# Optimization experiments

Hardware: AMD Instinct MI355X
Metric: run time of the kernel (lower is better)

## Reference

```python
import jax, jax.numpy as jnp
import numpy as np

N = 4096      # number of nodes
C = 8         # channels (w1..w8 in source)
IN_DIM = 256  # input feature dim
D = 64        # per-channel dim (c_dim)
OUT = 128     # out_dim
ITERS = 4     # routing iterations
BETA = 1.0    # temperature
DENSITY = 0.01


def _l2norm(x):
    # tf.nn.l2_normalize along last axis with eps=1e-12
    return x * jax.lax.rsqrt(jnp.maximum(jnp.sum(x * x, axis=-1, keepdims=True), 1e-12))


def setup_inputs() -> dict:
    key = jax.random.key(0)
    k0, k1, k2, k3, k4, k5 = jax.random.split(key, 6)
    features = jax.random.normal(k0, (N, IN_DIM), dtype=jnp.float32)
    # sparse-ish 0/1 adjacency stored densely (as in the original model)
    adj = (jax.random.uniform(k1, (N, N)) < DENSITY).astype(jnp.float32)
    W = jax.random.normal(k2, (C, IN_DIM, D), dtype=jnp.float32)    # w1..w8 stacked
    b = jax.random.normal(k3, (C, 1, D), dtype=jnp.float32)         # b1..b8 stacked
    W_o = jax.random.normal(k4, (C * D, OUT), dtype=jnp.float32)
    bias = jax.random.normal(k5, (1, OUT), dtype=jnp.float32)
    return {"features": features, "adj": adj, "W": W, "b": b, "W_o": W_o, "bias": bias}


def reference(features, adj, W, b, W_o, bias):
    mask = adj > 0  # [N, N]
    # per-channel projection + l2 normalize: z[c] = l2norm(features @ w[c] + b[c])
    z = _l2norm(jnp.einsum('ni,cid->cnd', features, W) + b)  # [C, N, D]
    for _ in range(ITERS):
        # dense per-channel attention (XX^T), masked by adjacency
        A = jnp.einsum('cnd,cmd->cnm', z, z)                 # [C, N, N]
        A = jnp.where(mask[None], A, 0.0) / BETA
        # softmax across channels at each (i, j), then re-mask
        A = jax.nn.softmax(A, axis=0)
        A = jnp.where(mask[None], A, 0.0)
        # aggregate + residual + l2 normalize
        z = _l2norm(z + jnp.einsum('cnm,cmd->cnd', A, z))
    # concat channels along feature axis: [N, C*D]
    h = jnp.transpose(z, (1, 0, 2)).reshape(N, C * D)
    # (dropout skipped: stochastic op, identity in the deterministic reference)
    return h @ W_o + bias
```

## Files before the change

### kernel.cpp

```cpp
#include <hip/hip_runtime.h>
#include <hip/hip_bf16.h>

#define N_NODES 4096
#define C_CH    8
#define IN_DIM  256
#define D_DIM   64
#define CD      512
#define OUT_DIM 128
#define ITERS   4
#define STRIDE  128

typedef __hip_bfloat16 bf16;
typedef short short8 __attribute__((ext_vector_type(8)));
typedef float floatx4 __attribute__((ext_vector_type(4)));

__device__ __forceinline__ float bf2f(bf16 x) { return __bfloat162float(x); }

__device__ __forceinline__ unsigned f2b_rne(float x) {
    unsigned u = __float_as_uint(x);
    return (u + 0x7FFFu + ((u >> 16) & 1u)) >> 16;
}
__device__ __forceinline__ unsigned pack2bf(float a, float b) {
    return f2b_rne(a) | (f2b_rne(b) << 16);
}
__device__ __forceinline__ void unpack2(unsigned v, float& a, float& b) {
    a = __uint_as_float(v << 16);
    b = __uint_as_float(v & 0xFFFF0000u);
}
__device__ __forceinline__ short8 as_s8(uint4 u) {
    union { uint4 a; short8 b; } x; x.a = u; return x.b;
}

template<int CTRL>
__device__ __forceinline__ float dpp_add(float x) {
    int yi = __builtin_amdgcn_update_dpp(0, __float_as_int(x), CTRL, 0xF, 0xF, true);
    return x + __int_as_float(yi);
}

__device__ __forceinline__ bool wave_detect(const unsigned* __restrict__ feat_u) {
    int lane = threadIdx.x & 63;
    unsigned u = feat_u[lane];
    int e = (u >> 7) & 0xFF;
    int vote = (e >= 0x68 && e <= 0x86) ? 1 : 0;
    #pragma unroll
    for (int off = 32; off; off >>= 1) vote += __shfl_xor(vote, off);
    return vote >= 32;
}

__global__ __launch_bounds__(256) void stage_a(
        const void* __restrict__ feat, const void* __restrict__ W,
        const void* __restrict__ Wo,
        unsigned short* __restrict__ Wt, unsigned short* __restrict__ Wo_t) {
    bool isbf = wave_detect((const unsigned*)feat);
    int bx = blockIdx.x, t = threadIdx.x;
    if (bx < 8) {
        __shared__ __align__(16) unsigned short lt[IN_DIM * D_DIM];
        int c = bx;
        if (isbf) {
            const uint4* p = (const uint4*)((const unsigned short*)W + (size_t)c * IN_DIM * D_DIM);
            #pragma unroll
            for (int i = 0; i < 8; i++) {
                int idx = t + i * 256;
                *(uint4*)&lt[idx * 8] = p[idx];
            }
        } else {
            const float4* p = (const float4*)((const float*)W + (size_t)c * IN_DIM * D_DIM);
            #pragma unroll
            for (int i = 0; i < 16; i++) {
                int idx = t + i * 256;
                float4 f = p[idx];
                uint2 v = make_uint2(pack2bf(f.x, f.y), pack2bf(f.z, f.w));
                *(uint2*)&lt[idx * 4] = v;
            }
        }
        __syncthreads();
        uint4* wt4 = (uint4*)Wt;
        #pragma unroll
        for (int i = 0; i < 8; i++) {
            int j = t + i * 256;
            int d = j >> 5, seg = j & 31;
            int k0 = seg * 8;
            unsigned short v[8];
            #pragma unroll
            for (int k = 0; k < 8; k++) v[k] = lt[(k0 + k) * D_DIM + d];
            uint4 o;
            o.x = v[0] | ((unsigned)v[1] << 16);
            o.y = v[2] | ((unsigned)v[3] << 16);
            o.z = v[4] | ((unsigned)v[5] << 16);
            o.w = v[6] | ((unsigned)v[7] << 16);
            wt4[(c * 64 + d) * 32 + seg] = o;
        }
    } else {
        int base = (bx - 8) * 1024 + t * 4;
        #pragma unroll
        for (int q = 0; q < 4; q++) {
            int idx = base + q;
            int k = idx >> 7, n = idx & 127;
            unsigned short v;
            if (isbf) v = ((const unsigned short*)Wo)[idx];
            else      v = (unsigned short)f2b_rne(((const float*)Wo)[idx]);
            Wo_t[n * CD + k] = v;
        }
    }
}

__global__ __launch_bounds__(256) void stage_b(
        const void* __restrict__ feat, const void* __restrict__ adj,
        const void* __restrict__ b, const unsigned short* __restrict__ Wt,
        unsigned* __restrict__ zbf, int* __restrict__ deg,
        int* __restrict__ col_buf) {
    bool isbf = wave_detect((const unsigned*)feat);
    int bx = blockIdx.x, t = threadIdx.x;
    int w = t >> 6, lane = t & 63;
    __shared__ __align__(16) unsigned short zt[16 * CD];

    if (bx < 256) {
        int r0 = bx * 16;
        int n0 = w * 128;
        int m = lane & 15, quad = lane >> 4;
        int row = r0 + m;
        floatx4 acc[8];
        #pragma unroll
        for (int j = 0; j < 8; j++) acc[j] = (floatx4){0.f, 0.f, 0.f, 0.f};
        const uint4* wt4 = (const uint4*)Wt;

        if (isbf) {
            const uint4* a4 = (const uint4*)feat + (size_t)row * 32 + quad;
            #pragma unroll
            for (int k0 = 0; k0 < 8; k0++) {
                short8 a = as_s8(a4[k0 * 4]);
                #pragma unroll
                for (int j = 0; j < 8; j++) {
                    int col = n0 + j * 16 + m;
                    short8 bb = as_s8(wt4[col * 32 + k0 * 4 + quad]);
                    acc[j] = __builtin_amdgcn_mfma_f32_16x16x32_bf16(a, bb, acc[j], 0, 0, 0);
                }
            }
        } else {
            const float4* a4 = (const float4*)feat + (size_t)row * 64 + quad * 2;
            #pragma unroll
            for (int k0 = 0; k0 < 8; k0++) {
                float4 f0 = a4[k0 * 8], f1 = a4[k0 * 8 + 1];
                uint4 au;
                au.x = pack2bf(f0.x, f0.y); au.y = pack2bf(f0.z, f0.w);
                au.z = pack2bf(f1.x, f1.y); au.w = pack2bf(f1.z, f1.w);
                short8 a = as_s8(au);
                #pragma unroll
                for (int j = 0; j < 8; j++) {
                    int col = n0 + j * 16 + m;
                    short8 bb = as_s8(wt4[col * 32 + k0 * 4 + quad]);
                    acc[j] = __builtin_amdgcn_mfma_f32_16x16x32_bf16(a, bb, acc[j], 0, 0, 0);
                }
            }
        }

        float pre[8][4];
        #pragma unroll
        for (int j = 0; j < 8; j++) {
            int col = n0 + j * 16 + m;
            float bb = isbf ? bf2f(((const bf16*)b)[col]) : ((const float*)b)[col];
            #pragma unroll
            for (int r = 0; r < 4; r++) pre[j][r] = acc[j][r] + bb;
        }
        #pragma unroll
        for (int ch = 0; ch < 2; ch++) {
            float ss[4];
            #pragma unroll
            for (int r = 0; r < 4; r++) {
                float s = 0.f;
                #pragma unroll
                for (int jj = 0; jj < 4; jj++) {
                    float v = pre[ch * 4 + jj][r];
                    s = fmaf(v, v, s);
                }
                ss[r] = s;
            }
            #pragma unroll
            for (int off = 1; off < 16; off <<= 1) {
                #pragma unroll
                for (int r = 0; r < 4; r++) ss[r] += __shfl_xor(ss[r], off);
            }
            #pragma unroll
            for (int r = 0; r < 4; r++) {
                float sc = __builtin_amdgcn_rsqf(fmaxf(ss[r], 1e-12f));
                int lrow = quad * 4 + r;
                #pragma unroll
                for (int jj = 0; jj < 4; jj++) {
                    int j = ch * 4 + jj;
                    int col = n0 + j * 16 + m;
                    zt[lrow * CD + col] = (unsigned short)f2b_rne(pre[j][r] * sc);
                }
            }
        }
        __syncthreads();
        const uint4* zt4 = (const uint4*)zt;
        uint4* z4 = (uint4*)zbf;
        #pragma unroll
        for (int i = 0; i < 4; i++) {
            int j = t + i * 256;
            int lrow = j >> 6, seg = j & 63;
            z4[(size_t)(r0 + lrow) * 64 + seg] = zt4[j];
        }
    } else {
        int i = (bx - 256) * 4 + w;
        int base_out = i * STRIDE;
        int running = 0;
        int nch = isbf ? 8 : 16;
        for (int ch = 0; ch < nch; ch++) {
            unsigned bits = 0;
            int j0, nelem;
            if (isbf) {
                const uint4* p = (const uint4*)((const unsigned short*)adj + (size_t)i * N_NODES);
                uint4 u = p[ch * 64 + lane];
                j0 = (ch * 64 + lane) * 8; nelem = 8;
                unsigned short h[8] = {
                    (unsigned short)(u.x & 0xFFFF), (unsigned short)(u.x >> 16),
                    (unsigned short)(u.y & 0xFFFF), (unsigned short)(u.y >> 16),
                    (unsigned short)(u.z & 0xFFFF), (unsigned short)(u.z >> 16),
                    (unsigned short)(u.w & 0xFFFF), (unsigned short)(u.w >> 16)};
                #pragma unroll
                for (int k = 0; k < 8; k++)
                    if ((h[k] & 0x8000) == 0 && h[k] != 0) bits |= (1u << k);
            } else {
                const float4* p = (const float4*)((const float*)adj + (size_t)i * N_NODES);
                float4 f = p[ch * 64 + lane];
                j0 = (ch * 64 + lane) * 4; nelem = 4;
                if (f.x > 0.f) bits |= 1u;
                if (f.y > 0.f) bits |= 2u;
                if (f.z > 0.f) bits |= 4u;
                if (f.w > 0.f) bits |= 8u;
            }
            int cnt = __popc(bits);
            int sc = cnt;
            #pragma unroll
            for (int off = 1; off < 64; off <<= 1) {
                int v = __shfl_up(sc, off);
                if (lane >= off) sc += v;
            }
            int tot = __shfl(sc, 63);
            int pos = base_out + running + (sc - cnt);
            for (int k = 0; k < nelem; k++) {
                if ((bits >> k) & 1u) {
                    if (pos < base_out + STRIDE) col_buf[pos] = j0 + k;
                    pos++;
                }
            }
            running += tot;
        }
        if (lane == 0) deg[i] = (running < STRIDE) ? running : STRIDE;
    }
}

__device__ __forceinline__ void edge_step(const float zi[8], float acc[8], uint4 u) {
    float vj[8];
    unpack2(u.x, vj[0], vj[1]);
    unpack2(u.y, vj[2], vj[3]);
    unpack2(u.z, vj[4], vj[5]);
    unpack2(u.w, vj[6], vj[7]);
    float p = 0.f;
    #pragma unroll
    for (int k = 0; k < 8; k++) p = fmaf(zi[k], vj[k], p);
    p = dpp_add<0xB1>(p);
    p = dpp_add<0x4E>(p);
    p = dpp_add<0x141>(p);
    float ex = __expf(p);
    float s = dpp_add<0x128>(ex);
    s += __shfl_xor(s, 16);
    s += __shfl_xor(s, 32);
    float wgt = ex * __builtin_amdgcn_rcpf(s);
    #pragma unroll
    for (int k = 0; k < 8; k++) acc[k] = fmaf(wgt, vj[k], acc[k]);
}

__global__ __launch_bounds__(256) void route_kernel(
        const unsigned* __restrict__ zbf_in, unsigned* __restrict__ zbf_out,
        const int* __restrict__ deg, const int* __restrict__ col_buf) {
    int t = threadIdx.x;
    int w = t >> 6, lane = t & 63;
    int i = blockIdx.x;
    int g = lane >> 3, s = lane & 7;
    __shared__ int   s_cols[STRIDE];
    __shared__ float s_acc[3][CD];
    if (t < STRIDE) s_cols[t] = col_buf[i * STRIDE + t];
    __syncthreads();

    int frag = g * 32 + s * 4;
    uint4 uown = *(const uint4*)(zbf_in + (size_t)i * 256 + frag);
    float zi[8], acc[8];
    unpack2(uown.x, zi[0], zi[1]); unpack2(uown.y, zi[2], zi[3]);
    unpack2(uown.z, zi[4], zi[5]); unpack2(uown.w, zi[6], zi[7]);
    #pragma unroll
    for (int k = 0; k < 8; k++) acc[k] = (w == 0) ? zi[k] : 0.f;

    int dg = deg[i];
    int e   = (dg * w) >> 2;
    int end = (dg * (w + 1)) >> 2;
    for (; e + 3 < end; e += 4) {
        int j0 = s_cols[e]     & (N_NODES - 1);
        int j1 = s_cols[e + 1] & (N_NODES - 1);
        int j2 = s_cols[e + 2] & (N_NODES - 1);
        int j3 = s_cols[e + 3] & (N_NODES - 1);
        uint4 u0 = *(const uint4*)(zbf_in + (size_t)j0 * 256 + frag);
        uint4 u1 = *(const uint4*)(zbf_in + (size_t)j1 * 256 + frag);
        uint4 u2 = *(const uint4*)(zbf_in + (size_t)j2 * 256 + frag);
        uint4 u3 = *(const uint4*)(zbf_in + (size_t)j3 * 256 + frag);
        edge_step(zi, acc, u0);
        edge_step(zi, acc, u1);
        edge_step(zi, acc, u2);
        edge_step(zi, acc, u3);
    }
    for (; e < end; e++) {
        int j0 = s_cols[e] & (N_NODES - 1);
        uint4 u0 = *(const uint4*)(zbf_in + (size_t)j0 * 256 + frag);
        edge_step(zi, acc, u0);
    }

    int flat = g * D_DIM + s * 8;
    if (w) {
        *(float4*)&s_acc[w - 1][flat]     = make_float4(acc[0], acc[1], acc[2], acc[3]);
        *(float4*)&s_acc[w - 1][flat + 4] = make_float4(acc[4], acc[5], acc[6], acc[7]);
    }
    __syncthreads();
    if (w == 0) {
        #pragma unroll
        for (int q = 0; q < 3; q++) {
            float4 p0 = *(const float4*)&s_acc[q][flat];
            float4 p1 = *(const float4*)&s_acc[q][flat + 4];
            acc[0] += p0.x; acc[1] += p0.y; acc[2] += p0.z; acc[3] += p0.w;
            acc[4] += p1.x; acc[5] += p1.y; acc[6] += p1.z; acc[7] += p1.w;
        }
        float ss = 0.f;
        #pragma unroll
        for (int k = 0; k < 8; k++) ss = fmaf(acc[k], acc[k], ss);
        ss = dpp_add<0xB1>(ss);
        ss = dpp_add<0x4E>(ss);
        ss = dpp_add<0x141>(ss);
        float sc = __builtin_amdgcn_rsqf(fmaxf(ss, 1e-12f));
        float o[8];
        #pragma unroll
        for (int k = 0; k < 8; k++) o[k] = acc[k] * sc;
        uint4 ob;
        ob.x = pack2bf(o[0], o[1]); ob.y = pack2bf(o[2], o[3]);
        ob.z = pack2bf(o[4], o[5]); ob.w = pack2bf(o[6], o[7]);
        *(uint4*)(zbf_out + (size_t)i * 256 + frag) = ob;
    }
}

__global__ __launch_bounds__(256) void out_gemm_mfma(
        const unsigned* __restrict__ zbf, const unsigned* __restrict__ wot_u,
        const void* __restrict__ bias, void* __restrict__ out,
        const void* __restrict__ feat) {
    bool isbf = wave_detect((const unsigned*)feat);
    int w = threadIdx.x >> 6, lane = threadIdx.x & 63;
    int r0 = blockIdx.x * 32 + (w & 1) * 16;
    int n0 = (w >> 1) * 64;
    int m = lane & 15, quad = lane >> 4;

    floatx4 acc0 = {0.f, 0.f, 0.f, 0.f}, acc1 = acc0, acc2 = acc0, acc3 = acc0;
    const unsigned* ap  = zbf   + (size_t)(r0 + m) * 256 + quad * 4;
    const unsigned* bp0 = wot_u + (size_t)(n0 + m) * 256 + quad * 4;
    const unsigned* bp1 = bp0 + 16 * 256;
    const unsigned* bp2 = bp0 + 32 * 256;
    const unsigned* bp3 = bp0 + 48 * 256;

    #pragma unroll
    for (int k0 = 0; k0 < 256; k0 += 16) {
        short8 a  = as_s8(*(const uint4*)(ap  + k0));
        short8 b0 = as_s8(*(const uint4*)(bp0 + k0));
        short8 b1 = as_s8(*(const uint4*)(bp1 + k0));
        short8 b2 = as_s8(*(const uint4*)(bp2 + k0));
        short8 b3 = as_s8(*(const uint4*)(bp3 + k0));
        acc0 = __builtin_amdgcn_mfma_f32_16x16x32_bf16(a, b0, acc0, 0, 0, 0);
        acc1 = __builtin_amdgcn_mfma_f32_16x16x32_bf16(a, b1, acc1, 0, 0, 0);
        acc2 = __builtin_amdgcn_mfma_f32_16x16x32_bf16(a, b2, acc2, 0, 0, 0);
        acc3 = __builtin_amdgcn_mfma_f32_16x16x32_bf16(a, b3, acc3, 0, 0, 0);
    }

    float accs[4][4] = {
        {acc0[0], acc0[1], acc0[2], acc0[3]},
        {acc1[0], acc1[1], acc1[2], acc1[3]},
        {acc2[0], acc2[1], acc2[2], acc2[3]},
        {acc3[0], acc3[1], acc3[2], acc3[3]}};
    #pragma unroll
    for (int c = 0; c < 4; c++) {
        int col = n0 + c * 16 + m;
        float bb = isbf ? bf2f(((const bf16*)bias)[col]) : ((const float*)bias)[col];
        #pragma unroll
        for (int r = 0; r < 4; r++) {
            int row = r0 + quad * 4 + r;
            float v = accs[c][r] + bb;
            size_t oi = (size_t)row * OUT_DIM + col;
            if (isbf) ((bf16*)out)[oi] = __float2bfloat16(v);
            else      ((float*)out)[oi] = v;
        }
    }
}

extern "C" void kernel_launch(void* const* d_in, const int* in_sizes, int n_in,
                              void* d_out, int out_size, void* d_ws, size_t ws_size,
                              hipStream_t stream) {
    const void* feat = d_in[0];
    const void* adj  = d_in[1];
    const void* W    = d_in[2];
    const void* b    = d_in[3];
    const void* Wo   = d_in[4];
    const void* bias = d_in[5];

    char* ws = (char*)d_ws;
    unsigned*       zbf_a   = (unsigned*)ws;
    unsigned*       zbf_b   = (unsigned*)(ws + (4u << 20));
    unsigned short* Wt      = (unsigned short*)(ws + (8u << 20));
    unsigned short* Wo_t    = (unsigned short*)(ws + (8u << 20) + (256u << 10));
    int*            deg     = (int*)(ws + (8u << 20) + (512u << 10));
    int*            col_buf = (int*)(ws + (9u << 20));

    stage_a<<<72, 256, 0, stream>>>(feat, W, Wo, Wt, Wo_t);
    stage_b<<<1280, 256, 0, stream>>>(feat, adj, b, Wt, zbf_a, deg, col_buf);

    unsigned* bin = zbf_a;
    unsigned* bot = zbf_b;
    for (int it = 0; it < ITERS; it++) {
        route_kernel<<<N_NODES, 256, 0, stream>>>(bin, bot, deg, col_buf);
        unsigned* tb = bin; bin = bot; bot = tb;
    }
    out_gemm_mfma<<<N_NODES / 32, 256, 0, stream>>>(zbf_a, (const unsigned*)Wo_t,
                                                    bias, d_out, feat);
}
```

Before: 206.1 us.

## Fuse routing iterations into one cooperative kernel with one node per wave

Replaces the four per-iteration route launches with a single cooperative kernel that keeps each node's vector in registers and uses grid-wide syncs between iterations, falling back to per-iteration launches when cooperative launch is not possible. Each wave now handles a whole node instead of four waves splitting one node's edges, which removes the shared-memory partial-sum reduction and the block barrier. It also switches exp to exp2 with a prescaled query and masks column indices once when they are loaded. The trade-offs are grid-sync cost and the occupancy limit (1024 blocks must be co-resident), plus load imbalance from per-node degree now falling on a single wave.

```diff
diff --git a/kernel.cpp b/kernel.cpp
--- a/kernel.cpp
+++ b/kernel.cpp
@@ -1,5 +1,8 @@
 #include <hip/hip_runtime.h>
 #include <hip/hip_bf16.h>
+#include <hip/hip_cooperative_groups.h>
+
+namespace cg = cooperative_groups;
 
 #define N_NODES 4096
 #define C_CH    8
@@ -251,7 +254,7 @@
     }
 }
 
-__device__ __forceinline__ void edge_step(const float zi[8], float acc[8], uint4 u) {
+__device__ __forceinline__ void edge_step(const float zil2[8], float acc[8], uint4 u) {
     float vj[8];
     unpack2(u.x, vj[0], vj[1]);
     unpack2(u.y, vj[2], vj[3]);
@@ -259,11 +262,11 @@
     unpack2(u.w, vj[6], vj[7]);
     float p = 0.f;
     #pragma unroll
-    for (int k = 0; k < 8; k++) p = fmaf(zi[k], vj[k], p);
+    for (int k = 0; k < 8; k++) p = fmaf(zil2[k], vj[k], p);
     p = dpp_add<0xB1>(p);
     p = dpp_add<0x4E>(p);
     p = dpp_add<0x141>(p);
-    float ex = __expf(p);
+    float ex = __builtin_amdgcn_exp2f(p);
     float s = dpp_add<0x128>(ex);
     s += __shfl_xor(s, 16);
     s += __shfl_xor(s, 32);
@@ -272,78 +275,125 @@
     for (int k = 0; k < 8; k++) acc[k] = fmaf(wgt, vj[k], acc[k]);
 }
 
-__global__ __launch_bounds__(256) void route_kernel(
-        const unsigned* __restrict__ zbf_in, unsigned* __restrict__ zbf_out,
+__device__ __forceinline__ void route_edges(const float zil2[8], float acc[8],
+        const char* __restrict__ bin, const int* __restrict__ mycols, int dg,
+        unsigned fragb) {
+    int e = 0;
+    for (; e + 3 < dg; e += 4) {
+        int4 js = *(const int4*)&mycols[e];
+        uint4 u0 = *(const uint4*)(bin + (((unsigned)js.x << 10) + fragb));
+        uint4 u1 = *(const uint4*)(bin + (((unsigned)js.y << 10) + fragb));
+        uint4 u2 = *(const uint4*)(bin + (((unsigned)js.z << 10) + fragb));
+        uint4 u3 = *(const uint4*)(bin + (((unsigned)js.w << 10) + fragb));
+        edge_step(zil2, acc, u0);
+        edge_step(zil2, acc, u1);
+        edge_step(zil2, acc, u2);
+        edge_step(zil2, acc, u3);
+    }
+    for (; e < dg; e++) {
+        uint4 u0 = *(const uint4*)(bin + (((unsigned)mycols[e] << 10) + fragb));
+        edge_step(zil2, acc, u0);
+    }
+}
+
+__device__ __forceinline__ void finish_norm(float acc[8], float zi[8]) {
+    float ss = 0.f;
+    #pragma unroll
+    for (int k = 0; k < 8; k++) ss = fmaf(acc[k], acc[k], ss);
+    ss = dpp_add<0xB1>(ss);
+    ss = dpp_add<0x4E>(ss);
+    ss = dpp_add<0x141>(ss);
+    float sc = __builtin_amdgcn_rsqf(fmaxf(ss, 1e-12f));
+    #pragma unroll
+    for (int k = 0; k < 8; k++) zi[k] = acc[k] * sc;
+}
+
+__global__ __launch_bounds__(256, 4) void route_coop(
+        unsigned* __restrict__ zbf_a, unsigned* __restrict__ zbf_b,
         const int* __restrict__ deg, const int* __restrict__ col_buf) {
+    const float LOG2E = 1.4426950408889634f;
     int t = threadIdx.x;
     int w = t >> 6, lane = t & 63;
-    int i = blockIdx.x;
+    int node = blockIdx.x * 4 + w;
     int g = lane >> 3, s = lane & 7;
-    __shared__ int   s_cols[STRIDE];
-    __shared__ float s_acc[3][CD];
-    if (t < STRIDE) s_cols[t] = col_buf[i * STRIDE + t];
+
+    __shared__ __align__(16) int s_cols[4 * STRIDE];
+    {
+        const int* src = col_buf + (size_t)blockIdx.x * (4 * STRIDE);
+        s_cols[t]       = src[t]       & (N_NODES - 1);
+        s_cols[t + 256] = src[t + 256] & (N_NODES - 1);
+    }
+    int dg = deg[node];
     __syncthreads();
+    const int* mycols = s_cols + w * STRIDE;
 
     int frag = g * 32 + s * 4;
-    uint4 uown = *(const uint4*)(zbf_in + (size_t)i * 256 + frag);
-    float zi[8], acc[8];
+    unsigned fragb = (unsigned)frag << 2;
+
+    uint4 uown = *(const uint4*)(zbf_a + (size_t)node * 256 + frag);
+    float zi[8];
     unpack2(uown.x, zi[0], zi[1]); unpack2(uown.y, zi[2], zi[3]);
     unpack2(uown.z, zi[4], zi[5]); unpack2(uown.w, zi[6], zi[7]);
-    #pragma unroll
-    for (int k = 0; k < 8; k++) acc[k] = (w == 0) ? zi[k] : 0.f;
-
-    int dg = deg[i];
-    int e   = (dg * w) >> 2;
-    int end = (dg * (w + 1)) >> 2;
-    for (; e + 3 < end; e += 4) {
-        int j0 = s_cols[e]     & (N_NODES - 1);
-        int j1 = s_cols[e + 1] & (N_NODES - 1);
-        int j2 = s_cols[e + 2] & (N_NODES - 1);
-        int j3 = s_cols[e + 3] & (N_NODES - 1);
-        uint4 u0 = *(const uint4*)(zbf_in + (size_t)j0 * 256 + frag);
-        uint4 u1 = *(const uint4*)(zbf_in + (size_t)j1 * 256 + frag);
-        uint4 u2 = *(const uint4*)(zbf_in + (size_t)j2 * 256 + frag);
-        uint4 u3 = *(const uint4*)(zbf_in + (size_t)j3 * 256 + frag);
-        edge_step(zi, acc, u0);
-        edge_step(zi, acc, u1);
-        edge_step(zi, acc, u2);
-        edge_step(zi, acc, u3);
-    }
-    for (; e < end; e++) {
-        int j0 = s_cols[e] & (N_NODES - 1);
-        uint4 u0 = *(const uint4*)(zbf_in + (size_t)j0 * 256 + frag);
-        edge_step(zi, acc, u0);
-    }
-
-    int flat = g * D_DIM + s * 8;
-    if (w) {
-        *(float4*)&s_acc[w - 1][flat]     = make_float4(acc[0], acc[1], acc[2], acc[3]);
-        *(float4*)&s_acc[w - 1][flat + 4] = make_float4(acc[4], acc[5], acc[6], acc[7]);
-    }
+
+    for (int it = 0; it < ITERS; it++) {
+        const char* bin = (const char*)((it & 1) ? zbf_b : zbf_a);
+        unsigned*   bot = (it & 1) ? zbf_a : zbf_b;
+
+        float zil2[8], acc[8];
+        #pragma unroll
+        for (int k = 0; k < 8; k++) { zil2[k] = zi[k] * LOG2E; acc[k] = zi[k]; }
+
+        route_edges(zil2, acc, bin, mycols, dg, fragb);
+        finish_norm(acc, zi);
+
+        uint4 ob;
+        ob.x = pack2bf(zi[0], zi[1]); ob.y = pack2bf(zi[2], zi[3]);
+        ob.z = pack2bf(zi[4], zi[5]); ob.w = pack2bf(zi[6], zi[7]);
+        *(uint4*)(bot + (size_t)node * 256 + frag) = ob;
+
+        if (it != ITERS - 1) {
+            __threadfence();
+            cg::this_grid().sync();
+        }
+    }
+}
+
+__global__ __launch_bounds__(256) void route_iter(
+        const unsigned* __restrict__ bin_u, unsigned* __restrict__ bot,
+        const int* __restrict__ deg, const int* __restrict__ col_buf) {
+    const float LOG2E = 1.4426950408889634f;
+    int t = threadIdx.x;
+    int w = t >> 6, lane = t & 63;
+    int node = blockIdx.x * 4 + w;
+    int g = lane >> 3, s = lane & 7;
+
+    __shared__ __align__(16) int s_cols[4 * STRIDE];
+    {
+        const int* src = col_buf + (size_t)blockIdx.x * (4 * STRIDE);
+        s_cols[t]       = src[t]       & (N_NODES - 1);
+        s_cols[t + 256] = src[t + 256] & (N_NODES - 1);
+    }
+    int dg = deg[node];
     __syncthreads();
-    if (w == 0) {
-        #pragma unroll
-        for (int q = 0; q < 3; q++) {
-            float4 p0 = *(const float4*)&s_acc[q][flat];
-            float4 p1 = *(const float4*)&s_acc[q][flat + 4];
-            acc[0] += p0.x; acc[1] += p0.y; acc[2] += p0.z; acc[3] += p0.w;
-            acc[4] += p1.x; acc[5] += p1.y; acc[6] += p1.z; acc[7] += p1.w;
-        }
-        float ss = 0.f;
-        #pragma unroll
-        for (int k = 0; k < 8; k++) ss = fmaf(acc[k], acc[k], ss);
-        ss = dpp_add<0xB1>(ss);
-        ss = dpp_add<0x4E>(ss);
-        ss = dpp_add<0x141>(ss);
-        float sc = __builtin_amdgcn_rsqf(fmaxf(ss, 1e-12f));
-        float o[8];
-        #pragma unroll
-        for (int k = 0; k < 8; k++) o[k] = acc[k] * sc;
-        uint4 ob;
-        ob.x = pack2bf(o[0], o[1]); ob.y = pack2bf(o[2], o[3]);
-        ob.z = pack2bf(o[4], o[5]); ob.w = pack2bf(o[6], o[7]);
-        *(uint4*)(zbf_out + (size_t)i * 256 + frag) = ob;
-    }
+    const int* mycols = s_cols + w * STRIDE;
+
+    int frag = g * 32 + s * 4;
+    unsigned fragb = (unsigned)frag << 2;
+
+    uint4 uown = *(const uint4*)(bin_u + (size_t)node * 256 + frag);
+    float zi[8], zil2[8], acc[8];
+    unpack2(uown.x, zi[0], zi[1]); unpack2(uown.y, zi[2], zi[3]);
+    unpack2(uown.z, zi[4], zi[5]); unpack2(uown.w, zi[6], zi[7]);
+    #pragma unroll
+    for (int k = 0; k < 8; k++) { zil2[k] = zi[k] * LOG2E; acc[k] = zi[k]; }
+
+    route_edges(zil2, acc, (const char*)bin_u, mycols, dg, fragb);
+    finish_norm(acc, zi);
+
+    uint4 ob;
+    ob.x = pack2bf(zi[0], zi[1]); ob.y = pack2bf(zi[2], zi[3]);
+    ob.z = pack2bf(zi[4], zi[5]); ob.w = pack2bf(zi[6], zi[7]);
+    *(uint4*)(bot + (size_t)node * 256 + frag) = ob;
 }
 
 __global__ __launch_bounds__(256) void out_gemm_mfma(
@@ -417,12 +467,29 @@
     stage_a<<<72, 256, 0, stream>>>(feat, W, Wo, Wt, Wo_t);
     stage_b<<<1280, 256, 0, stream>>>(feat, adj, b, Wt, zbf_a, deg, col_buf);
 
-    unsigned* bin = zbf_a;
-    unsigned* bot = zbf_b;
-    for (int it = 0; it < ITERS; it++) {
-        route_kernel<<<N_NODES, 256, 0, stream>>>(bin, bot, deg, col_buf);
-        unsigned* tb = bin; bin = bot; bot = tb;
-    }
+    bool coop_done = false;
+    {
+        int nb = 0;
+        hipError_t oe = hipOccupancyMaxActiveBlocksPerMultiprocessor(
+                &nb, route_coop, 256, 0);
+        if (oe == hipSuccess && nb >= 4) {
+            void* args[4] = {(void*)&zbf_a, (void*)&zbf_b, (void*)&deg,
+                             (void*)&col_buf};
+            hipError_t le = hipLaunchCooperativeKernel(
+                    reinterpret_cast<void*>(route_coop),
+                    dim3(N_NODES / 4), dim3(256), args, 0, stream);
+            coop_done = (le == hipSuccess);
+        }
+    }
+    if (!coop_done) {
+        unsigned* bin = zbf_a;
+        unsigned* bot = zbf_b;
+        for (int it = 0; it < ITERS; it++) {
+            route_iter<<<N_NODES / 4, 256, 0, stream>>>(bin, bot, deg, col_buf);
+            unsigned* tb = bin; bin = bot; bot = tb;
+        }
+    }
+
     out_gemm_mfma<<<N_NODES / 32, 256, 0, stream>>>(zbf_a, (const unsigned*)Wo_t,
                                                     bias, d_out, feat);
 }
```

Result: slower. 213.6 us (+3.6%).

## Route two nodes per block with two waves each and exp2-based softmax

Applied to the files above, without the earlier changes.

Restructures the routing kernel so each 256-thread block handles two nodes, with two waves splitting each node's edge list instead of four waves on one node. This halves the cross-wave reduction through shared memory and the grid size. It also pre-masks the column indices once, loads four indices as one int4, and uses byte-offset addressing. The exp is replaced with exp2 on inputs prescaled by log2e, and the launch bounds request higher occupancy. Each node now gets less edge-level parallelism, so latency per node may rise, and the 8-aligned split may leave the two waves with uneven work.

```diff
diff --git a/kernel.cpp b/kernel.cpp
--- a/kernel.cpp
+++ b/kernel.cpp
@@ -251,7 +251,7 @@
     }
 }
 
-__device__ __forceinline__ void edge_step(const float zi[8], float acc[8], uint4 u) {
+__device__ __forceinline__ void edge_step(const float zil2[8], float acc[8], uint4 u) {
     float vj[8];
     unpack2(u.x, vj[0], vj[1]);
     unpack2(u.y, vj[2], vj[3]);
@@ -259,11 +259,11 @@
     unpack2(u.w, vj[6], vj[7]);
     float p = 0.f;
     #pragma unroll
-    for (int k = 0; k < 8; k++) p = fmaf(zi[k], vj[k], p);
+    for (int k = 0; k < 8; k++) p = fmaf(zil2[k], vj[k], p);
     p = dpp_add<0xB1>(p);
     p = dpp_add<0x4E>(p);
     p = dpp_add<0x141>(p);
-    float ex = __expf(p);
+    float ex = __builtin_amdgcn_exp2f(p);
     float s = dpp_add<0x128>(ex);
     s += __shfl_xor(s, 16);
     s += __shfl_xor(s, 32);
@@ -272,77 +272,89 @@
     for (int k = 0; k < 8; k++) acc[k] = fmaf(wgt, vj[k], acc[k]);
 }
 
-__global__ __launch_bounds__(256) void route_kernel(
-        const unsigned* __restrict__ zbf_in, unsigned* __restrict__ zbf_out,
+__device__ __forceinline__ void finish_norm(float acc[8], float zi[8]) {
+    float ss = 0.f;
+    #pragma unroll
+    for (int k = 0; k < 8; k++) ss = fmaf(acc[k], acc[k], ss);
+    ss = dpp_add<0xB1>(ss);
+    ss = dpp_add<0x4E>(ss);
+    ss = dpp_add<0x141>(ss);
+    float sc = __builtin_amdgcn_rsqf(fmaxf(ss, 1e-12f));
+    #pragma unroll
+    for (int k = 0; k < 8; k++) zi[k] = acc[k] * sc;
+}
+
+__global__ __launch_bounds__(256, 8) void route_iter(
+        const unsigned* __restrict__ bin_u, unsigned* __restrict__ bot,
         const int* __restrict__ deg, const int* __restrict__ col_buf) {
+    const float LOG2E = 1.4426950408889634f;
     int t = threadIdx.x;
     int w = t >> 6, lane = t & 63;
-    int i = blockIdx.x;
+    int local = w >> 1;
+    int half  = w & 1;
+    int node = blockIdx.x * 2 + local;
     int g = lane >> 3, s = lane & 7;
-    __shared__ int   s_cols[STRIDE];
-    __shared__ float s_acc[3][CD];
-    if (t < STRIDE) s_cols[t] = col_buf[i * STRIDE + t];
+
+    __shared__ __align__(16) int   s_cols[2 * STRIDE];
+    __shared__ __align__(16) float s_acc[2][CD];
+    s_cols[t] = col_buf[(size_t)blockIdx.x * (2 * STRIDE) + t] & (N_NODES - 1);
+    int dg = deg[node];
     __syncthreads();
+    const int* mycols = s_cols + local * STRIDE;
 
     int frag = g * 32 + s * 4;
-    uint4 uown = *(const uint4*)(zbf_in + (size_t)i * 256 + frag);
-    float zi[8], acc[8];
+    unsigned fragb = (unsigned)frag << 2;
+
+    uint4 uown = *(const uint4*)(bin_u + (size_t)node * 256 + frag);
+    float zi[8], zil2[8], acc[8];
     unpack2(uown.x, zi[0], zi[1]); unpack2(uown.y, zi[2], zi[3]);
     unpack2(uown.z, zi[4], zi[5]); unpack2(uown.w, zi[6], zi[7]);
     #pragma unroll
-    for (int k = 0; k < 8; k++) acc[k] = (w == 0) ? zi[k] : 0.f;
-
-    int dg = deg[i];
-    int e   = (dg * w) >> 2;
-    int end = (dg * (w + 1)) >> 2;
+    for (int k = 0; k < 8; k++) {
+        zil2[k] = zi[k] * LOG2E;
+        acc[k] = half ? 0.f : zi[k];
+    }
+
+    int h0 = ((dg >> 1) + 7) & ~7;
+    if (h0 > dg) h0 = dg;
+    int e   = half ? h0 : 0;
+    int end = half ? dg : h0;
+
+    const char* bin = (const char*)bin_u;
     for (; e + 3 < end; e += 4) {
-        int j0 = s_cols[e]     & (N_NODES - 1);
-        int j1 = s_cols[e + 1] & (N_NODES - 1);
-        int j2 = s_cols[e + 2] & (N_NODES - 1);
-        int j3 = s_cols[e + 3] & (N_NODES - 1);
-        uint4 u0 = *(const uint4*)(zbf_in + (size_t)j0 * 256 + frag);
-        uint4 u1 = *(const uint4*)(zbf_in + (size_t)j1 * 256 + frag);
-        uint4 u2 = *(const uint4*)(zbf_in + (size_t)j2 * 256 + frag);
-        uint4 u3 = *(const uint4*)(zbf_in + (size_t)j3 * 256 + frag);
-        edge_step(zi, acc, u0);
-        edge_step(zi, acc, u1);
-        edge_step(zi, acc, u2);
-        edge_step(zi, acc, u3);
+        int4 js = *(const int4*)&mycols[e];
+        uint4 u0 = *(const uint4*)(bin + (((unsigned)js.x << 10) + fragb));
+        uint4 u1 = *(const uint4*)(bin + (((unsigned)js.y << 10) + fragb));
+        uint4 u2 = *(const uint4*)(bin + (((unsigned)js.z << 10) + fragb));
+        uint4 u3 = *(const uint4*)(bin + (((unsigned)js.w << 10) + fragb));
+        edge_step(zil2, acc, u0);
+        edge_step(zil2, acc, u1);
+        edge_step(zil2, acc, u2);
+        edge_step(zil2, acc, u3);
     }
     for (; e < end; e++) {
-        int j0 = s_cols[e] & (N_NODES - 1);
-        uint4 u0 = *(const uint4*)(zbf_in + (size_t)j0 * 256 + frag);
-        edge_step(zi, acc, u0);
+        uint4 u0 = *(const uint4*)(bin + (((unsigned)mycols[e] << 10) + fragb));
+        edge_step(zil2, acc, u0);
     }
 
     int flat = g * D_DIM + s * 8;
-    if (w) {
-        *(float4*)&s_acc[w - 1][flat]     = make_float4(acc[0], acc[1], acc[2], acc[3]);
-        *(float4*)&s_acc[w - 1][flat + 4] = make_float4(acc[4], acc[5], acc[6], acc[7]);
+    if (half) {
+        *(float4*)&s_acc[local][flat]     = make_float4(acc[0], acc[1], acc[2], acc[3]);
+        *(float4*)&s_acc[local][flat + 4] = make_float4(acc[4], acc[5], acc[6], acc[7]);
     }
     __syncthreads();
-    if (w == 0) {
-        #pragma unroll
-        for (int q = 0; q < 3; q++) {
-            float4 p0 = *(const float4*)&s_acc[q][flat];
-            float4 p1 = *(const float4*)&s_acc[q][flat + 4];
-            acc[0] += p0.x; acc[1] += p0.y; acc[2] += p0.z; acc[3] += p0.w;
-            acc[4] += p1.x; acc[5] += p1.y; acc[6] += p1.z; acc[7] += p1.w;
-        }
-        float ss = 0.f;
-        #pragma unroll
-        for (int k = 0; k < 8; k++) ss = fmaf(acc[k], acc[k], ss);
-        ss = dpp_add<0xB1>(ss);
-        ss = dpp_add<0x4E>(ss);
-        ss = dpp_add<0x141>(ss);
-        float sc = __builtin_amdgcn_rsqf(fmaxf(ss, 1e-12f));
-        float o[8];
-        #pragma unroll
-        for (int k = 0; k < 8; k++) o[k] = acc[k] * sc;
+    if (!half) {
+        float4 p0 = *(const float4*)&s_acc[local][flat];
+        float4 p1 = *(const float4*)&s_acc[local][flat + 4];
+        acc[0] += p0.x; acc[1] += p0.y; acc[2] += p0.z; acc[3] += p0.w;
+        acc[4] += p1.x; acc[5] += p1.y; acc[6] += p1.z; acc[7] += p1.w;
+
+        finish_norm(acc, zi);
+
         uint4 ob;
-        ob.x = pack2bf(o[0], o[1]); ob.y = pack2bf(o[2], o[3]);
-        ob.z = pack2bf(o[4], o[5]); ob.w = pack2bf(o[6], o[7]);
-        *(uint4*)(zbf_out + (size_t)i * 256 + frag) = ob;
+        ob.x = pack2bf(zi[0], zi[1]); ob.y = pack2bf(zi[2], zi[3]);
+        ob.z = pack2bf(zi[4], zi[5]); ob.w = pack2bf(zi[6], zi[7]);
+        *(uint4*)(bot + (size_t)node * 256 + frag) = ob;
     }
 }
 
@@ -420,9 +432,10 @@
     unsigned* bin = zbf_a;
     unsigned* bot = zbf_b;
     for (int it = 0; it < ITERS; it++) {
-        route_kernel<<<N_NODES, 256, 0, stream>>>(bin, bot, deg, col_buf);
+        route_iter<<<N_NODES / 2, 256, 0, stream>>>(bin, bot, deg, col_buf);
         unsigned* tb = bin; bin = bot; bot = tb;
     }
+
     out_gemm_mfma<<<N_NODES / 32, 256, 0, stream>>>(zbf_a, (const unsigned*)Wo_t,
                                                     bias, d_out, feat);
 }
```

After: 208.4 us. Within noise of the previous version (+1.1%).
